# Kernel optimization log

Hardware: AMD Instinct MI355X
Metric: run time of the kernel (lower is better)

## Reference

```python
import jax, jax.numpy as jnp
import numpy as np

C = 1.0
TOP_K = 5
TAU = 0.1
NEG_SAMPLES = 20
EPS = 1e-9

B, D = 8192, 64


def setup_inputs() -> dict:
    key = jax.random.key(0)
    x = jax.random.normal(key, (B, D), dtype=jnp.float32)
    # scale into the Poincare ball (||x|| < 1)
    x = 0.9 * x / (1.0 + jnp.linalg.norm(x, axis=-1, keepdims=True))
    return {"embeds": x}


def _pairwise_poincare_distance(x):
    # ||xi - xj||^2 = ||xi||^2 + ||xj||^2 - 2 xi.xj  (same math as explicit diff,
    # avoids the [B,B,D] intermediate)
    norm_sq = jnp.sum(x * x, axis=-1)                      # [B]
    gram = x @ x.T                                          # [B,B]
    diff_norm_sq = jnp.maximum(norm_sq[:, None] + norm_sq[None, :] - 2.0 * gram, 0.0)
    ns_cl = jnp.minimum(norm_sq, 1.0 - EPS)
    denom = jnp.maximum((1.0 - ns_cl)[:, None] * (1.0 - ns_cl)[None, :], EPS)
    z = jnp.maximum(1.0 + 2.0 * diff_norm_sq / denom, 1.0 + EPS)
    return jnp.arccosh(z) / jnp.sqrt(jnp.float32(C))


def reference(embeds):
    n = embeds.shape[0]
    dist = _pairwise_poincare_distance(embeds)
    dist = jnp.where(jnp.eye(n, dtype=bool), jnp.inf, dist)

    k = min(TOP_K, n - 1)
    neg_vals, pos_idx = jax.lax.top_k(-dist, k)            # smallest k distances
    pos_dist = -neg_vals                                    # [B,k]
    pos_term = jax.nn.logsumexp(-pos_dist / TAU, axis=1)    # [B]

    rows = jnp.arange(n)[:, None]
    mask = jnp.ones((n, n), dtype=bool).at[rows, pos_idx].set(False)
    # indices of True (allowed) entries, per row; each row has exactly n-k True
    pool_idx = jnp.argsort(~mask, axis=1, stable=True)[:, : n - k]   # [B, n-k]

    skey = jax.random.key(42)
    samp = jax.random.randint(skey, (n, NEG_SAMPLES), 0, n - k)
    cols = jnp.take_along_axis(pool_idx, samp, axis=1)      # [B, neg_samples]
    neg_pool = jnp.take_along_axis(dist, cols, axis=1)      # [B, neg_samples]
    neg_term = jax.nn.logsumexp(-neg_pool / TAU, axis=1)    # [B]

    loss = -(pos_term - neg_term)
    return jnp.mean(loss)
```

## Files before the change

kernel.cpp:

```cpp
#include <hip/hip_runtime.h>
#include <cstdint>
#include <cstddef>

typedef _Float16 f16x8 __attribute__((ext_vector_type(8)));
typedef float f32x4 __attribute__((ext_vector_type(4)));

#define N_ROWS 8192
#define SPAN   8187u
#define MULT   1600u
#define TAU_INV 10.0f
#define TOTAL_SAMP 163840u
#define INIT32 0xFFFFFFFFu

__device__ __forceinline__ void tf_round(unsigned &x0, unsigned &x1, int r) {
    x0 += x1; x1 = (x1 << r) | (x1 >> (32 - r)); x1 ^= x0;
}
__device__ __forceinline__ void threefry2x32(unsigned k0, unsigned k1,
                                             unsigned c0, unsigned c1,
                                             unsigned &o0, unsigned &o1) {
    unsigned ks2 = k0 ^ k1 ^ 0x1BD11BDAu;
    unsigned x0 = c0 + k0, x1 = c1 + k1;
    tf_round(x0, x1, 13); tf_round(x0, x1, 15); tf_round(x0, x1, 26); tf_round(x0, x1, 6);
    x0 += k1;  x1 += ks2 + 1u;
    tf_round(x0, x1, 17); tf_round(x0, x1, 29); tf_round(x0, x1, 16); tf_round(x0, x1, 24);
    x0 += ks2; x1 += k0 + 2u;
    tf_round(x0, x1, 13); tf_round(x0, x1, 15); tf_round(x0, x1, 26); tf_round(x0, x1, 6);
    x0 += k0;  x1 += k1 + 3u;
    tf_round(x0, x1, 17); tf_round(x0, x1, 29); tf_round(x0, x1, 16); tf_round(x0, x1, 24);
    x0 += k1;  x1 += ks2 + 4u;
    tf_round(x0, x1, 13); tf_round(x0, x1, 15); tf_round(x0, x1, 26); tf_round(x0, x1, 6);
    x0 += ks2; x1 += k0 + 5u;
    o0 = x0; o1 = x1;
}

__device__ __forceinline__ void async16(void* lds, const void* g) {
    __builtin_amdgcn_global_load_lds((const __attribute__((address_space(1))) void*)g,
                                     (__attribute__((address_space(3))) void*)lds, 16, 0, 0);
}

__device__ __forceinline__ void stage_chunk(char* lds_tile, const char* gtile, int q, int lane) {
    int off16 = (q << 6) + lane;
    int r = off16 >> 3;
    int slot = off16 & 7;
    int csrc = slot ^ (r & 7);
    async16(lds_tile + (q << 10), gtile + r * 128 + (csrc << 4));
}

__device__ __forceinline__ f16x8 read_frag(const char* tile, int row, int c) {
    return *(const f16x8*)(tile + row * 128 + (((c ^ (row & 7)) << 4)));
}

__device__ __forceinline__ unsigned umed3(unsigned a, unsigned b, unsigned c) {
    unsigned d;
    asm("v_med3_u32 %0, %1, %2, %3" : "=v"(d) : "v"(a), "v"(b), "v"(c));
    return d;
}

__device__ __forceinline__ float wave_maxf(float v) {
#pragma unroll
    for (int o = 32; o; o >>= 1) v = fmaxf(v, __shfl_xor(v, o));
    return v;
}
__device__ __forceinline__ float wave_sumf(float v) {
#pragma unroll
    for (int o = 32; o; o >>= 1) v += __shfl_xor(v, o);
    return v;
}
__device__ __forceinline__ unsigned wave_minu32(unsigned v) {
#pragma unroll
    for (int o = 32; o; o >>= 1) {
        unsigned w = (unsigned)__shfl_xor((int)v, o);
        v = (w < v) ? w : v;
    }
    return v;
}
__device__ __forceinline__ unsigned group_minu32(unsigned v) {
#pragma unroll
    for (int o = 8; o; o >>= 1) {
        unsigned w = (unsigned)__shfl_xor((int)v, o);
        v = (w < v) ? w : v;
    }
    return v;
}

__global__ void prep_kernel(const float* __restrict__ X,
                            float2* __restrict__ nsiv,
                            char* __restrict__ Xf) {
    int t = blockIdx.x * 256 + threadIdx.x;
    int row = t >> 3, c = t & 7;
    const float4* src = (const float4*)(X + (size_t)row * 64 + c * 8);
    float4 a = src[0], b = src[1];
    float v[8] = {a.x, a.y, a.z, a.w, b.x, b.y, b.z, b.w};
    float ss = 0.f;
#pragma unroll
    for (int j = 0; j < 8; ++j) ss = fmaf(v[j], v[j], ss);
    ss += __shfl_xor(ss, 1);
    ss += __shfl_xor(ss, 2);
    ss += __shfl_xor(ss, 4);
    f16x8 h;
#pragma unroll
    for (int j = 0; j < 8; ++j) h[j] = (_Float16)v[j];
    *(f16x8*)(Xf + (size_t)row * 128 + c * 16) = h;
    if (c == 0) nsiv[row] = make_float2(ss, 1.0f / (1.0f - fminf(ss, 1.0f)));
}

__global__ __launch_bounds__(256, 3) void gram_topk(
        const char* __restrict__ Xf,
        const float2* __restrict__ nsiv, unsigned* __restrict__ part) {
    __shared__ __align__(16) char lds[16384];

    const int t = threadIdx.x, lane = t & 63, wv = t >> 6;
    const int lx = lane & 15, lq = lane >> 4;
    const int r0 = (blockIdx.x >> 5) * 128;
    const int ch = blockIdx.x & 31;
    const int j0base = ch * 256;

    const char* gA = Xf + (size_t)r0 * 128;
#pragma unroll
    for (int q = 0; q < 4; ++q) stage_chunk(lds, gA, 4 * wv + q, lane);
    __syncthreads();

    f16x8 a0f[2], a1f[2];
#pragma unroll
    for (int kc = 0; kc < 2; ++kc) {
        a0f[kc] = read_frag(lds, wv * 32 +      lx, kc * 4 + lq);
        a1f[kc] = read_frag(lds, wv * 32 + 16 + lx, kc * 4 + lq);
    }
    __syncthreads();

    stage_chunk(lds, Xf + (size_t)j0base * 128, 2 * wv, lane);
    stage_chunk(lds, Xf + (size_t)j0base * 128, 2 * wv + 1, lane);

    const char* pB0 = lds + lx * 128 + ((lq       ^ (lx & 7)) << 4);
    const char* pB1 = lds + lx * 128 + (((4 + lq) ^ (lx & 7)) << 4);
    const int rA  = 16 * wv + (lane >> 3);
    const int csA = (lane & 7) ^ ((lane >> 3) & 7);
    const char* gb = Xf + (size_t)(j0base + 64) * 128 + rA * 128 + (csA << 4);
    const float2* pn = nsiv + j0base + lx;
    const int jlx = j0base + lx;

    int gm0[4], gm1[4]; float rns0[4], rns1[4];
#pragma unroll
    for (int r = 0; r < 4; ++r) {
        int gr = r0 + wv * 32 + lq * 4 + r;
        gm0[r] = gr - jlx;
        gm1[r] = gr + 16 - jlx;
        rns0[r] = nsiv[gr].x;
        rns1[r] = nsiv[gr + 16].x;
    }

    unsigned tk0[4][5], tk1[4][5];
#pragma unroll
    for (int r = 0; r < 4; ++r)
#pragma unroll
        for (int s = 0; s < 5; ++s) { tk0[r][s] = INIT32; tk1[r][s] = INIT32; }

    int itofs = 0;
    __syncthreads();

#define INS5(TK, KK)                                                          \
    TK[4] = umed3(TK[3], TK[4], KK);                                          \
    TK[3] = umed3(TK[2], TK[3], KK);                                          \
    TK[2] = umed3(TK[1], TK[2], KK);                                          \
    TK[1] = umed3(TK[0], TK[1], KK);                                          \
    TK[0] = (KK < TK[0]) ? KK : TK[0];

#define ITER(SEL, NSEL, DO_STAGE) do {                                        \
    if (DO_STAGE) {                                                           \
        async16(lds + (NSEL) + wv * 2048,        gb);                         \
        async16(lds + (NSEL) + wv * 2048 + 1024, gb + 1024);                  \
        gb += 8192;                                                           \
    }                                                                         \
    float2 cnv[4] = {pn[0], pn[16], pn[32], pn[48]};                          \
    pn += 64;                                                                 \
    _Pragma("unroll")                                                         \
    for (int ct = 0; ct < 4; ++ct) {                                          \
        const f16x8 bh0 = *(const f16x8*)(pB0 + (SEL) + ct * 2048);           \
        const f16x8 bh1 = *(const f16x8*)(pB1 + (SEL) + ct * 2048);           \
        f32x4 a0 = {0.f, 0.f, 0.f, 0.f};                                      \
        f32x4 a1 = {0.f, 0.f, 0.f, 0.f};                                      \
        a0 = __builtin_amdgcn_mfma_f32_16x16x32_f16(a0f[0], bh0, a0, 0,0,0);  \
        a1 = __builtin_amdgcn_mfma_f32_16x16x32_f16(a1f[0], bh0, a1, 0,0,0);  \
        a0 = __builtin_amdgcn_mfma_f32_16x16x32_f16(a0f[1], bh1, a0, 0,0,0);  \
        a1 = __builtin_amdgcn_mfma_f32_16x16x32_f16(a1f[1], bh1, a1, 0,0,0);  \
        const float civ    = cnv[ct].y;                                       \
        const float cnsciv = cnv[ct].x * civ;                                 \
        const float m2civ  = -2.0f * civ;                                     \
        const unsigned gcol = (unsigned)(jlx + itofs + ct * 16);              \
        const int dofs = itofs + ct * 16;                                     \
        _Pragma("unroll")                                                     \
        for (int r = 0; r < 4; ++r) {                                         \
            float q0 = fmaf(a0[r], m2civ, fmaf(rns0[r], civ, cnsciv));        \
            q0 = fmaxf(q0, 0.0f);                                             \
            unsigned k0 = (__float_as_uint(q0) & 0xFFFFE000u) | gcol;         \
            k0 = (gm0[r] == dofs) ? INIT32 : k0;                              \
            INS5(tk0[r], k0)                                                  \
            float q1 = fmaf(a1[r], m2civ, fmaf(rns1[r], civ, cnsciv));        \
            q1 = fmaxf(q1, 0.0f);                                             \
            unsigned k1 = (__float_as_uint(q1) & 0xFFFFE000u) | gcol;         \
            k1 = (gm1[r] == dofs) ? INIT32 : k1;                              \
            INS5(tk1[r], k1)                                                  \
        }                                                                     \
    }                                                                         \
    itofs += 64;                                                              \
    __syncthreads();                                                          \
} while (0)

#pragma unroll 1
    for (int ip = 0; ip < 2; ++ip) {
        ITER(0, 8192, true);
        ITER(8192, 0, ip < 1);
    }
#undef ITER
#undef INS5

#define MERGE(TK, GM) do {                                                    \
    _Pragma("unroll")                                                         \
    for (int r = 0; r < 4; ++r) {                                             \
        unsigned t5r[5];                                                      \
        _Pragma("unroll")                                                     \
        for (int s = 0; s < 5; ++s) t5r[s] = TK[r][s];                        \
        unsigned out = INIT32;                                                \
        unsigned h = t5r[0];                                                  \
        _Pragma("unroll")                                                     \
        for (int s = 0; s < 5; ++s) {                                         \
            unsigned m = group_minu32(h);                                     \
            if (lx == s) out = m;                                             \
            if (h == m) {                                                     \
                t5r[0] = t5r[1]; t5r[1] = t5r[2]; t5r[2] = t5r[3];            \
                t5r[3] = t5r[4]; t5r[4] = INIT32;                             \
                h = t5r[0];                                                   \
            }                                                                 \
        }                                                                     \
        if (lx < 5) part[(size_t)(GM[r] + jlx) * 160 + (size_t)ch * 5 + lx] = out; \
    }                                                                         \
} while (0)

    MERGE(tk0, gm0);
    MERGE(tk1, gm1);
#undef MERGE
}

__global__ __launch_bounds__(256) void finalize_kernel(
        const float* __restrict__ X, const float2* __restrict__ nsiv,
        const unsigned* __restrict__ part, float* __restrict__ out) {
    const int t = threadIdx.x, lane = t & 63, wv = t >> 6;

    float wsum = 0.f;
#pragma unroll 1
    for (int rr = 0; rr < 4; ++rr) {
        const int row = blockIdx.x * 16 + wv * 4 + rr;

        const unsigned* prow = part + (size_t)row * 160;
        unsigned ka = prow[lane];
        unsigned kb = prow[64 + lane];
        unsigned kc = (lane < 32) ? prow[128 + lane] : INIT32;
        unsigned s0 = (ka < kb) ? ka : kb;
        unsigned s1 = (ka < kb) ? kb : ka;
        unsigned r0 = (s0 < kc) ? s0 : kc;
        unsigned tm = (s0 < kc) ? kc : s0;
        unsigned r1 = (s1 < tm) ? s1 : tm;
        unsigned r2 = (s1 < tm) ? tm : s1;
        unsigned b[5];
#pragma unroll
        for (int s = 0; s < 5; ++s) {
            unsigned m = wave_minu32(r0);
            b[s] = m;
            if (r0 == m) { r0 = r1; r1 = r2; r2 = INIT32; }
        }

        int pcol[5], ids[5];
#pragma unroll
        for (int s = 0; s < 5; ++s) { pcol[s] = (int)(b[s] & 8191u); ids[s] = pcol[s]; }
        for (int i = 0; i < 4; ++i)
            for (int j = 0; j < 4 - i; ++j)
                if (ids[j] > ids[j + 1]) { int tmp = ids[j]; ids[j] = ids[j + 1]; ids[j + 1] = tmp; }

        int col = row;
        if (lane < 20) {
            unsigned m0 = (unsigned)(row * 20 + lane);
            unsigned hi, lo;
            threefry2x32(0u, 42u, m0, m0 + TOTAL_SAMP, hi, lo);
            unsigned samp = ((hi % SPAN) * MULT + (lo % SPAN)) % SPAN;
            int c = (int)samp;
#pragma unroll
            for (int s = 0; s < 5; ++s) c += (ids[s] <= c) ? 1 : 0;
            col = c;
        } else if (lane < 25) {
            col = pcol[lane - 20];
        }

        float term = -INFINITY;
        if (lane < 25 && col != row) {
            const float4* xr = (const float4*)(X + (size_t)row * 64);
            const float4* xc = (const float4*)(X + (size_t)col * 64);
            float dot = 0.f;
#pragma unroll
            for (int k = 0; k < 16; ++k) {
                float4 a = xr[k];
                float4 c = xc[k];
                dot = fmaf(a.x, c.x, dot);
                dot = fmaf(a.y, c.y, dot);
                dot = fmaf(a.z, c.z, dot);
                dot = fmaf(a.w, c.w, dot);
            }
            float nsi = nsiv[row].x, nsj = nsiv[col].x;
            float d2  = fmaxf(nsi + nsj - 2.f * dot, 0.f);
            float ci  = 1.f - fminf(nsi, 1.f);
            float cj  = 1.f - fminf(nsj, 1.f);
            float den = fmaxf(ci * cj, 1e-9f);
            float z   = fmaxf(1.f + 2.f * d2 / den, 1.f);
            term = -acoshf(z) * TAU_INV;
        }

        float negt = (lane < 20) ? term : -INFINITY;
        float post = (lane >= 20 && lane < 25) ? term : -INFINITY;

        float nm = wave_maxf(negt);
        float ne = (lane < 20 && negt != -INFINITY) ? expf(negt - nm) : 0.f;
        float neg = nm + logf(wave_sumf(ne));

        float pm = wave_maxf(post);
        float pe = (lane >= 20 && lane < 25) ? expf(post - pm) : 0.f;
        float pos = pm + logf(wave_sumf(pe));

        if (lane == 0) wsum += neg - pos;
    }

    __shared__ float ws4[4];
    if (lane == 0) ws4[wv] = wsum;
    __syncthreads();
    if (t == 0)
        atomicAdd(out, (ws4[0] + ws4[1] + ws4[2] + ws4[3]) * (1.0f / 8192.0f));
}

extern "C" void kernel_launch(void* const* d_in, const int* in_sizes, int n_in,
                              void* d_out, int out_size, void* d_ws, size_t ws_size,
                              hipStream_t stream) {
    (void)in_sizes; (void)n_in; (void)out_size; (void)ws_size;
    const float* X = (const float*)d_in[0];
    float* out = (float*)d_out;

    float2*   nsiv = (float2*)d_ws;
    char*     Xf   = (char*)d_ws + 65536;
    unsigned* part = (unsigned*)((char*)d_ws + 65536 + 1048576);

    prep_kernel<<<256, 256, 0, stream>>>(X, nsiv, Xf);
    gram_topk<<<2048, 256, 0, stream>>>(Xf, nsiv, part);
    finalize_kernel<<<512, 256, 0, stream>>>(X, nsiv, part, out);
}
```

Baseline: 120.1 us.

## Specialize diagonal-free tiles and restructure finalize reduction with counter-based last-block write

The gram/top-k loop is split into two instantiations so that tiles not touching the diagonal skip the per-element self-distance masking compare. The finalize kernel now gives each wave one row in 1024-thread blocks instead of looping over four rows per wave in 256-thread blocks. It also replaces a direct atomicAdd into the output with partial sums spread over eight slots plus a completion counter, and the last block writes the mean. This removes the need for a pre-zeroed output and reduces atomic contention on one address, at the cost of zeroing workspace in the prep kernel and a threadfence handshake.

```diff
diff --git a/kernel.cpp b/kernel.cpp
--- a/kernel.cpp
+++ b/kernel.cpp
@@ -85,7 +85,13 @@
 
 __global__ void prep_kernel(const float* __restrict__ X,
                             float2* __restrict__ nsiv,
-                            char* __restrict__ Xf) {
+                            char* __restrict__ Xf,
+                            float* __restrict__ ws8,
+                            unsigned* __restrict__ cnt) {
+    if (blockIdx.x == 0 && threadIdx.x < 9) {
+        if (threadIdx.x < 8) ws8[threadIdx.x] = 0.f;
+        else *cnt = 0u;
+    }
     int t = blockIdx.x * 256 + threadIdx.x;
     int row = t >> 3, c = t & 7;
     const float4* src = (const float4*)(X + (size_t)row * 64 + c * 8);
@@ -165,7 +171,7 @@
     TK[1] = umed3(TK[0], TK[1], KK);                                          \
     TK[0] = (KK < TK[0]) ? KK : TK[0];
 
-#define ITER(SEL, NSEL, DO_STAGE) do {                                        \
+#define ITER(SEL, NSEL, DO_STAGE, DIAG) do {                                  \
     if (DO_STAGE) {                                                           \
         async16(lds + (NSEL) + wv * 2048,        gb);                         \
         async16(lds + (NSEL) + wv * 2048 + 1024, gb + 1024);                  \
@@ -188,17 +194,18 @@
         const float m2civ  = -2.0f * civ;                                     \
         const unsigned gcol = (unsigned)(jlx + itofs + ct * 16);              \
         const int dofs = itofs + ct * 16;                                     \
+        (void)dofs;                                                           \
         _Pragma("unroll")                                                     \
         for (int r = 0; r < 4; ++r) {                                         \
             float q0 = fmaf(a0[r], m2civ, fmaf(rns0[r], civ, cnsciv));        \
             q0 = fmaxf(q0, 0.0f);                                             \
             unsigned k0 = (__float_as_uint(q0) & 0xFFFFE000u) | gcol;         \
-            k0 = (gm0[r] == dofs) ? INIT32 : k0;                              \
+            if (DIAG) k0 = (gm0[r] == dofs) ? INIT32 : k0;                    \
             INS5(tk0[r], k0)                                                  \
             float q1 = fmaf(a1[r], m2civ, fmaf(rns1[r], civ, cnsciv));        \
             q1 = fmaxf(q1, 0.0f);                                             \
             unsigned k1 = (__float_as_uint(q1) & 0xFFFFE000u) | gcol;         \
-            k1 = (gm1[r] == dofs) ? INIT32 : k1;                              \
+            if (DIAG) k1 = (gm1[r] == dofs) ? INIT32 : k1;                    \
             INS5(tk1[r], k1)                                                  \
         }                                                                     \
     }                                                                         \
@@ -206,10 +213,19 @@
     __syncthreads();                                                          \
 } while (0)
 
+    const bool hasdiag = (r0 < j0base + 256) && (j0base < r0 + 128);
+    if (hasdiag) {
 #pragma unroll 1
-    for (int ip = 0; ip < 2; ++ip) {
-        ITER(0, 8192, true);
-        ITER(8192, 0, ip < 1);
+        for (int ip = 0; ip < 2; ++ip) {
+            ITER(0, 8192, true, 1);
+            ITER(8192, 0, ip < 1, 1);
+        }
+    } else {
+#pragma unroll 1
+        for (int ip = 0; ip < 2; ++ip) {
+            ITER(0, 8192, true, 0);
+            ITER(8192, 0, ip < 1, 0);
+        }
     }
 #undef ITER
 #undef INS5
@@ -241,97 +257,103 @@
 #undef MERGE
 }
 
-__global__ __launch_bounds__(256) void finalize_kernel(
+__global__ __launch_bounds__(1024) void finalize_kernel(
         const float* __restrict__ X, const float2* __restrict__ nsiv,
-        const unsigned* __restrict__ part, float* __restrict__ out) {
+        const unsigned* __restrict__ part, float* __restrict__ ws8,
+        unsigned* __restrict__ cnt, float* __restrict__ out) {
     const int t = threadIdx.x, lane = t & 63, wv = t >> 6;
-
-    float wsum = 0.f;
-#pragma unroll 1
-    for (int rr = 0; rr < 4; ++rr) {
-        const int row = blockIdx.x * 16 + wv * 4 + rr;
-
-        const unsigned* prow = part + (size_t)row * 160;
-        unsigned ka = prow[lane];
-        unsigned kb = prow[64 + lane];
-        unsigned kc = (lane < 32) ? prow[128 + lane] : INIT32;
-        unsigned s0 = (ka < kb) ? ka : kb;
-        unsigned s1 = (ka < kb) ? kb : ka;
-        unsigned r0 = (s0 < kc) ? s0 : kc;
-        unsigned tm = (s0 < kc) ? kc : s0;
-        unsigned r1 = (s1 < tm) ? s1 : tm;
-        unsigned r2 = (s1 < tm) ? tm : s1;
-        unsigned b[5];
-#pragma unroll
-        for (int s = 0; s < 5; ++s) {
-            unsigned m = wave_minu32(r0);
-            b[s] = m;
-            if (r0 == m) { r0 = r1; r1 = r2; r2 = INIT32; }
+    const int row = blockIdx.x * 16 + wv;
+
+    const unsigned* prow = part + (size_t)row * 160;
+    unsigned ka = prow[lane];
+    unsigned kb = prow[64 + lane];
+    unsigned kc = (lane < 32) ? prow[128 + lane] : INIT32;
+    unsigned s0 = (ka < kb) ? ka : kb;
+    unsigned s1 = (ka < kb) ? kb : ka;
+    unsigned r0 = (s0 < kc) ? s0 : kc;
+    unsigned tm = (s0 < kc) ? kc : s0;
+    unsigned r1 = (s1 < tm) ? s1 : tm;
+    unsigned r2 = (s1 < tm) ? tm : s1;
+    unsigned b[5];
+#pragma unroll
+    for (int s = 0; s < 5; ++s) {
+        unsigned m = wave_minu32(r0);
+        b[s] = m;
+        if (r0 == m) { r0 = r1; r1 = r2; r2 = INIT32; }
+    }
+
+    int pcol[5], ids[5];
+#pragma unroll
+    for (int s = 0; s < 5; ++s) { pcol[s] = (int)(b[s] & 8191u); ids[s] = pcol[s]; }
+    for (int i = 0; i < 4; ++i)
+        for (int j = 0; j < 4 - i; ++j)
+            if (ids[j] > ids[j + 1]) { int tmp = ids[j]; ids[j] = ids[j + 1]; ids[j + 1] = tmp; }
+
+    int col = row;
+    if (lane < 20) {
+        unsigned m0 = (unsigned)(row * 20 + lane);
+        unsigned hi, lo;
+        threefry2x32(0u, 42u, m0, m0 + TOTAL_SAMP, hi, lo);
+        unsigned samp = ((hi % SPAN) * MULT + (lo % SPAN)) % SPAN;
+        int c = (int)samp;
+#pragma unroll
+        for (int s = 0; s < 5; ++s) c += (ids[s] <= c) ? 1 : 0;
+        col = c;
+    } else if (lane < 25) {
+        col = pcol[lane - 20];
+    }
+
+    float term = -INFINITY;
+    if (lane < 25 && col != row) {
+        const float4* xr = (const float4*)(X + (size_t)row * 64);
+        const float4* xc = (const float4*)(X + (size_t)col * 64);
+        float dot = 0.f;
+#pragma unroll
+        for (int k = 0; k < 16; ++k) {
+            float4 a = xr[k];
+            float4 c = xc[k];
+            dot = fmaf(a.x, c.x, dot);
+            dot = fmaf(a.y, c.y, dot);
+            dot = fmaf(a.z, c.z, dot);
+            dot = fmaf(a.w, c.w, dot);
         }
-
-        int pcol[5], ids[5];
-#pragma unroll
-        for (int s = 0; s < 5; ++s) { pcol[s] = (int)(b[s] & 8191u); ids[s] = pcol[s]; }
-        for (int i = 0; i < 4; ++i)
-            for (int j = 0; j < 4 - i; ++j)
-                if (ids[j] > ids[j + 1]) { int tmp = ids[j]; ids[j] = ids[j + 1]; ids[j + 1] = tmp; }
-
-        int col = row;
-        if (lane < 20) {
-            unsigned m0 = (unsigned)(row * 20 + lane);
-            unsigned hi, lo;
-            threefry2x32(0u, 42u, m0, m0 + TOTAL_SAMP, hi, lo);
-            unsigned samp = ((hi % SPAN) * MULT + (lo % SPAN)) % SPAN;
-            int c = (int)samp;
-#pragma unroll
-            for (int s = 0; s < 5; ++s) c += (ids[s] <= c) ? 1 : 0;
-            col = c;
-        } else if (lane < 25) {
-            col = pcol[lane - 20];
+        float nsi = nsiv[row].x, nsj = nsiv[col].x;
+        float d2  = fmaxf(nsi + nsj - 2.f * dot, 0.f);
+        float ci  = 1.f - fminf(nsi, 1.f);
+        float cj  = 1.f - fminf(nsj, 1.f);
+        float den = fmaxf(ci * cj, 1e-9f);
+        float z   = fmaxf(1.f + 2.f * d2 / den, 1.f);
+        term = -acoshf(z) * TAU_INV;
+    }
+
+    float negt = (lane < 20) ? term : -INFINITY;
+    float post = (lane >= 20 && lane < 25) ? term : -INFINITY;
+
+    float nm = wave_maxf(negt);
+    float ne = (lane < 20 && negt != -INFINITY) ? expf(negt - nm) : 0.f;
+    float neg = nm + logf(wave_sumf(ne));
+
+    float pm = wave_maxf(post);
+    float pe = (lane >= 20 && lane < 25) ? expf(post - pm) : 0.f;
+    float pos = pm + logf(wave_sumf(pe));
+
+    __shared__ float ws16[16];
+    if (lane == 0) ws16[wv] = neg - pos;
+    __syncthreads();
+    if (t == 0) {
+        float s = 0.f;
+#pragma unroll
+        for (int i = 0; i < 16; ++i) s += ws16[i];
+        atomicAdd(&ws8[blockIdx.x & 7], s);
+        __threadfence();
+        unsigned old = atomicAdd(cnt, 1u);
+        if (old == 511u) {
+            float tot = 0.f;
+#pragma unroll
+            for (int i = 0; i < 8; ++i) tot += atomicAdd(&ws8[i], 0.0f);
+            out[0] = tot * (1.0f / 8192.0f);
         }
-
-        float term = -INFINITY;
-        if (lane < 25 && col != row) {
-            const float4* xr = (const float4*)(X + (size_t)row * 64);
-            const float4* xc = (const float4*)(X + (size_t)col * 64);
-            float dot = 0.f;
-#pragma unroll
-            for (int k = 0; k < 16; ++k) {
-                float4 a = xr[k];
-                float4 c = xc[k];
-                dot = fmaf(a.x, c.x, dot);
-                dot = fmaf(a.y, c.y, dot);
-                dot = fmaf(a.z, c.z, dot);
-                dot = fmaf(a.w, c.w, dot);
-            }
-            float nsi = nsiv[row].x, nsj = nsiv[col].x;
-            float d2  = fmaxf(nsi + nsj - 2.f * dot, 0.f);
-            float ci  = 1.f - fminf(nsi, 1.f);
-            float cj  = 1.f - fminf(nsj, 1.f);
-            float den = fmaxf(ci * cj, 1e-9f);
-            float z   = fmaxf(1.f + 2.f * d2 / den, 1.f);
-            term = -acoshf(z) * TAU_INV;
-        }
-
-        float negt = (lane < 20) ? term : -INFINITY;
-        float post = (lane >= 20 && lane < 25) ? term : -INFINITY;
-
-        float nm = wave_maxf(negt);
-        float ne = (lane < 20 && negt != -INFINITY) ? expf(negt - nm) : 0.f;
-        float neg = nm + logf(wave_sumf(ne));
-
-        float pm = wave_maxf(post);
-        float pe = (lane >= 20 && lane < 25) ? expf(post - pm) : 0.f;
-        float pos = pm + logf(wave_sumf(pe));
-
-        if (lane == 0) wsum += neg - pos;
-    }
-
-    __shared__ float ws4[4];
-    if (lane == 0) ws4[wv] = wsum;
-    __syncthreads();
-    if (t == 0)
-        atomicAdd(out, (ws4[0] + ws4[1] + ws4[2] + ws4[3]) * (1.0f / 8192.0f));
+    }
 }
 
 extern "C" void kernel_launch(void* const* d_in, const int* in_sizes, int n_in,
@@ -344,8 +366,10 @@
     float2*   nsiv = (float2*)d_ws;
     char*     Xf   = (char*)d_ws + 65536;
     unsigned* part = (unsigned*)((char*)d_ws + 65536 + 1048576);
-
-    prep_kernel<<<256, 256, 0, stream>>>(X, nsiv, Xf);
+    float*    ws8  = (float*)((char*)d_ws + 65536 + 1048576 + 5242880);
+    unsigned* cnt  = (unsigned*)((char*)d_ws + 65536 + 1048576 + 5242880 + 32);
+
+    prep_kernel<<<256, 256, 0, stream>>>(X, nsiv, Xf, ws8, cnt);
     gram_topk<<<2048, 256, 0, stream>>>(Xf, nsiv, part);
-    finalize_kernel<<<512, 256, 0, stream>>>(X, nsiv, part, out);
-}
+    finalize_kernel<<<512, 1024, 0, stream>>>(X, nsiv, part, ws8, cnt, out);
+}
```

Measured after the change: 126.8 us. +5.6%, slower.

## Triple-buffer column tiles, widen column chunks, and split final reduction into separate kernel

Applied to the files above, without the earlier changes.

The gram_topk kernel now gives each block 512 columns instead of 256, halving the grid and the partial top-k candidates per row (80 instead of 160). B tiles are staged through a three-buffer LDS ring with explicit vmcnt waits and raw barriers in place of the two-buffer __syncthreads scheme. Column norms are staged into LDS asynchronously. The finalize kernel uses one wave per row and writes per-row losses, and a new single-block reduce kernel replaces the atomicAdd. The goal is to hide global load latency and cut merge and finalize work, at the cost of more LDS per block, which may lower occupancy, and an extra kernel launch.

```diff
diff --git a/kernel.cpp b/kernel.cpp
--- a/kernel.cpp
+++ b/kernel.cpp
@@ -107,17 +107,19 @@
 __global__ __launch_bounds__(256, 3) void gram_topk(
         const char* __restrict__ Xf,
         const float2* __restrict__ nsiv, unsigned* __restrict__ part) {
-    __shared__ __align__(16) char lds[16384];
+    __shared__ __align__(16) char lds[29696];
 
     const int t = threadIdx.x, lane = t & 63, wv = t >> 6;
     const int lx = lane & 15, lq = lane >> 4;
-    const int r0 = (blockIdx.x >> 5) * 128;
-    const int ch = blockIdx.x & 31;
-    const int j0base = ch * 256;
+    const int r0 = (blockIdx.x >> 4) * 128;
+    const int ch = blockIdx.x & 15;
+    const int j0base = ch * 512;
 
     const char* gA = Xf + (size_t)r0 * 128;
 #pragma unroll
     for (int q = 0; q < 4; ++q) stage_chunk(lds, gA, 4 * wv + q, lane);
+    async16(lds + 24576 + wv * 1024, (const char*)(nsiv + j0base) + wv * 1024 + lane * 16);
+    if (wv == 0) async16(lds + 28672, (const char*)(nsiv + r0) + lane * 16);
     __syncthreads();
 
     f16x8 a0f[2], a1f[2];
@@ -126,28 +128,30 @@
         a0f[kc] = read_frag(lds, wv * 32 +      lx, kc * 4 + lq);
         a1f[kc] = read_frag(lds, wv * 32 + 16 + lx, kc * 4 + lq);
     }
+    const float2* rowns = (const float2*)(lds + 28672);
+    float rns0[4], rns1[4];
+#pragma unroll
+    for (int r = 0; r < 4; ++r) {
+        rns0[r] = rowns[wv * 32 + lq * 4 + r].x;
+        rns1[r] = rowns[wv * 32 + lq * 4 + r + 16].x;
+    }
+    const int jlx = j0base + lx;
+    const int dg  = (r0 + wv * 32 + lq * 4) - jlx;
     __syncthreads();
 
-    stage_chunk(lds, Xf + (size_t)j0base * 128, 2 * wv, lane);
-    stage_chunk(lds, Xf + (size_t)j0base * 128, 2 * wv + 1, lane);
-
-    const char* pB0 = lds + lx * 128 + ((lq       ^ (lx & 7)) << 4);
-    const char* pB1 = lds + lx * 128 + (((4 + lq) ^ (lx & 7)) << 4);
     const int rA  = 16 * wv + (lane >> 3);
     const int csA = (lane & 7) ^ ((lane >> 3) & 7);
-    const char* gb = Xf + (size_t)(j0base + 64) * 128 + rA * 128 + (csA << 4);
-    const float2* pn = nsiv + j0base + lx;
-    const int jlx = j0base + lx;
-
-    int gm0[4], gm1[4]; float rns0[4], rns1[4];
-#pragma unroll
-    for (int r = 0; r < 4; ++r) {
-        int gr = r0 + wv * 32 + lq * 4 + r;
-        gm0[r] = gr - jlx;
-        gm1[r] = gr + 16 - jlx;
-        rns0[r] = nsiv[gr].x;
-        rns1[r] = nsiv[gr + 16].x;
-    }
+    const char* gb = Xf + (size_t)j0base * 128 + rA * 128 + (csA << 4);
+    async16(lds +        wv * 2048,        gb);
+    async16(lds +        wv * 2048 + 1024, gb + 1024);
+    gb += 8192;
+    async16(lds + 8192 + wv * 2048,        gb);
+    async16(lds + 8192 + wv * 2048 + 1024, gb + 1024);
+    gb += 8192;
+
+    const char* pB0  = lds + lx * 128 + ((lq       ^ (lx & 7)) << 4);
+    const char* pB1  = lds + lx * 128 + (((4 + lq) ^ (lx & 7)) << 4);
+    const char* pnlp = lds + 24576 + lx * 8;
 
     unsigned tk0[4][5], tk1[4][5];
 #pragma unroll
@@ -156,7 +160,6 @@
         for (int s = 0; s < 5; ++s) { tk0[r][s] = INIT32; tk1[r][s] = INIT32; }
 
     int itofs = 0;
-    __syncthreads();
 
 #define INS5(TK, KK)                                                          \
     TK[4] = umed3(TK[3], TK[4], KK);                                          \
@@ -165,26 +168,31 @@
     TK[1] = umed3(TK[0], TK[1], KK);                                          \
     TK[0] = (KK < TK[0]) ? KK : TK[0];
 
-#define ITER(SEL, NSEL, DO_STAGE) do {                                        \
+#define ITER(RSEL, SSEL, DO_STAGE, VMSTR) do {                                \
+    asm volatile("" ::: "memory");                                            \
+    __builtin_amdgcn_s_barrier();      \
+    asm volatile("" ::: "memory");                                            \
     if (DO_STAGE) {                                                           \
-        async16(lds + (NSEL) + wv * 2048,        gb);                         \
-        async16(lds + (NSEL) + wv * 2048 + 1024, gb + 1024);                  \
+        async16(lds + (SSEL) + wv * 2048,        gb);                         \
+        async16(lds + (SSEL) + wv * 2048 + 1024, gb + 1024);                  \
         gb += 8192;                                                           \
     }                                                                         \
-    float2 cnv[4] = {pn[0], pn[16], pn[32], pn[48]};                          \
-    pn += 64;                                                                 \
+    asm volatile("s_waitcnt vmcnt(" VMSTR ")" ::: "memory");                  \
+    __builtin_amdgcn_s_barrier();      \
+    asm volatile("" ::: "memory");                                            \
     _Pragma("unroll")                                                         \
     for (int ct = 0; ct < 4; ++ct) {                                          \
-        const f16x8 bh0 = *(const f16x8*)(pB0 + (SEL) + ct * 2048);           \
-        const f16x8 bh1 = *(const f16x8*)(pB1 + (SEL) + ct * 2048);           \
+        const f16x8 bh0 = *(const f16x8*)(pB0 + (RSEL) + ct * 2048);          \
+        const f16x8 bh1 = *(const f16x8*)(pB1 + (RSEL) + ct * 2048);          \
         f32x4 a0 = {0.f, 0.f, 0.f, 0.f};                                      \
         f32x4 a1 = {0.f, 0.f, 0.f, 0.f};                                      \
         a0 = __builtin_amdgcn_mfma_f32_16x16x32_f16(a0f[0], bh0, a0, 0,0,0);  \
         a1 = __builtin_amdgcn_mfma_f32_16x16x32_f16(a1f[0], bh0, a1, 0,0,0);  \
         a0 = __builtin_amdgcn_mfma_f32_16x16x32_f16(a0f[1], bh1, a0, 0,0,0);  \
         a1 = __builtin_amdgcn_mfma_f32_16x16x32_f16(a1f[1], bh1, a1, 0,0,0);  \
-        const float civ    = cnv[ct].y;                                       \
-        const float cnsciv = cnv[ct].x * civ;                                 \
+        const float2 cn = *(const float2*)(pnlp + ct * 128);                  \
+        const float civ    = cn.y;                                            \
+        const float cnsciv = cn.x * civ;                                      \
         const float m2civ  = -2.0f * civ;                                     \
         const unsigned gcol = (unsigned)(jlx + itofs + ct * 16);              \
         const int dofs = itofs + ct * 16;                                     \
@@ -193,28 +201,32 @@
             float q0 = fmaf(a0[r], m2civ, fmaf(rns0[r], civ, cnsciv));        \
             q0 = fmaxf(q0, 0.0f);                                             \
             unsigned k0 = (__float_as_uint(q0) & 0xFFFFE000u) | gcol;         \
-            k0 = (gm0[r] == dofs) ? INIT32 : k0;                              \
+            k0 = (dofs - r == dg) ? INIT32 : k0;                              \
             INS5(tk0[r], k0)                                                  \
             float q1 = fmaf(a1[r], m2civ, fmaf(rns1[r], civ, cnsciv));        \
             q1 = fmaxf(q1, 0.0f);                                             \
             unsigned k1 = (__float_as_uint(q1) & 0xFFFFE000u) | gcol;         \
-            k1 = (gm1[r] == dofs) ? INIT32 : k1;                              \
+            k1 = (dofs - r - 16 == dg) ? INIT32 : k1;                         \
             INS5(tk1[r], k1)                                                  \
         }                                                                     \
     }                                                                         \
     itofs += 64;                                                              \
-    __syncthreads();                                                          \
+    pnlp  += 512;                                                             \
+    asm volatile("" ::: "memory");                                            \
 } while (0)
 
 #pragma unroll 1
     for (int ip = 0; ip < 2; ++ip) {
-        ITER(0, 8192, true);
-        ITER(8192, 0, ip < 1);
-    }
+        ITER(0,     16384, true, "4");
+        ITER(8192,  0,     true, "4");
+        ITER(16384, 8192,  true, "4");
+    }
+    ITER(0,    0, false, "2");
+    ITER(8192, 0, false, "0");
 #undef ITER
 #undef INS5
 
-#define MERGE(TK, GM) do {                                                    \
+#define MERGE(TK, ROWOFS) do {                                                \
     _Pragma("unroll")                                                         \
     for (int r = 0; r < 4; ++r) {                                             \
         unsigned t5r[5];                                                      \
@@ -232,106 +244,105 @@
                 h = t5r[0];                                                   \
             }                                                                 \
         }                                                                     \
-        if (lx < 5) part[(size_t)(GM[r] + jlx) * 160 + (size_t)ch * 5 + lx] = out; \
+        if (lx < 5)                                                           \
+            part[(size_t)(r0 + wv * 32 + lq * 4 + r + (ROWOFS)) * 80          \
+                 + (size_t)ch * 5 + lx] = out;                                \
     }                                                                         \
 } while (0)
 
-    MERGE(tk0, gm0);
-    MERGE(tk1, gm1);
+    MERGE(tk0, 0);
+    MERGE(tk1, 16);
 #undef MERGE
 }
 
 __global__ __launch_bounds__(256) void finalize_kernel(
         const float* __restrict__ X, const float2* __restrict__ nsiv,
-        const unsigned* __restrict__ part, float* __restrict__ out) {
+        const unsigned* __restrict__ part, float* __restrict__ rowloss) {
     const int t = threadIdx.x, lane = t & 63, wv = t >> 6;
-
-    float wsum = 0.f;
-#pragma unroll 1
-    for (int rr = 0; rr < 4; ++rr) {
-        const int row = blockIdx.x * 16 + wv * 4 + rr;
-
-        const unsigned* prow = part + (size_t)row * 160;
-        unsigned ka = prow[lane];
-        unsigned kb = prow[64 + lane];
-        unsigned kc = (lane < 32) ? prow[128 + lane] : INIT32;
-        unsigned s0 = (ka < kb) ? ka : kb;
-        unsigned s1 = (ka < kb) ? kb : ka;
-        unsigned r0 = (s0 < kc) ? s0 : kc;
-        unsigned tm = (s0 < kc) ? kc : s0;
-        unsigned r1 = (s1 < tm) ? s1 : tm;
-        unsigned r2 = (s1 < tm) ? tm : s1;
-        unsigned b[5];
-#pragma unroll
-        for (int s = 0; s < 5; ++s) {
-            unsigned m = wave_minu32(r0);
-            b[s] = m;
-            if (r0 == m) { r0 = r1; r1 = r2; r2 = INIT32; }
+    const int row = blockIdx.x * 4 + wv;
+
+    const unsigned* prow = part + (size_t)row * 80;
+    unsigned a0 = prow[lane];
+    unsigned a1 = (lane < 16) ? prow[64 + lane] : INIT32;
+    unsigned klo = (a0 < a1) ? a0 : a1;
+    unsigned khi = (a0 < a1) ? a1 : a0;
+    unsigned b[5];
+#pragma unroll
+    for (int s = 0; s < 5; ++s) {
+        unsigned m = wave_minu32(klo);
+        b[s] = m;
+        if (klo == m) { klo = khi; khi = INIT32; }
+    }
+
+    int pcol[5], ids[5];
+#pragma unroll
+    for (int s = 0; s < 5; ++s) { pcol[s] = (int)(b[s] & 8191u); ids[s] = pcol[s]; }
+    for (int i = 0; i < 4; ++i)
+        for (int j = 0; j < 4 - i; ++j)
+            if (ids[j] > ids[j + 1]) { int tmp = ids[j]; ids[j] = ids[j + 1]; ids[j + 1] = tmp; }
+
+    int col = row;
+    if (lane < 20) {
+        unsigned m0 = (unsigned)(row * 20 + lane);
+        unsigned hi, lo;
+        threefry2x32(0u, 42u, m0, m0 + TOTAL_SAMP, hi, lo);
+        unsigned samp = ((hi % SPAN) * MULT + (lo % SPAN)) % SPAN;
+        int c = (int)samp;
+#pragma unroll
+        for (int s = 0; s < 5; ++s) c += (ids[s] <= c) ? 1 : 0;
+        col = c;
+    } else if (lane < 25) {
+        col = pcol[lane - 20];
+    }
+
+    float term = -INFINITY;
+    if (lane < 25 && col != row) {
+        const float4* xr = (const float4*)(X + (size_t)row * 64);
+        const float4* xc = (const float4*)(X + (size_t)col * 64);
+        float dot = 0.f;
+#pragma unroll
+        for (int k = 0; k < 16; ++k) {
+            float4 a = xr[k];
+            float4 c = xc[k];
+            dot = fmaf(a.x, c.x, dot);
+            dot = fmaf(a.y, c.y, dot);
+            dot = fmaf(a.z, c.z, dot);
+            dot = fmaf(a.w, c.w, dot);
         }
-
-        int pcol[5], ids[5];
-#pragma unroll
-        for (int s = 0; s < 5; ++s) { pcol[s] = (int)(b[s] & 8191u); ids[s] = pcol[s]; }
-        for (int i = 0; i < 4; ++i)
-            for (int j = 0; j < 4 - i; ++j)
-                if (ids[j] > ids[j + 1]) { int tmp = ids[j]; ids[j] = ids[j + 1]; ids[j + 1] = tmp; }
-
-        int col = row;
-        if (lane < 20) {
-            unsigned m0 = (unsigned)(row * 20 + lane);
-            unsigned hi, lo;
-            threefry2x32(0u, 42u, m0, m0 + TOTAL_SAMP, hi, lo);
-            unsigned samp = ((hi % SPAN) * MULT + (lo % SPAN)) % SPAN;
-            int c = (int)samp;
-#pragma unroll
-            for (int s = 0; s < 5; ++s) c += (ids[s] <= c) ? 1 : 0;
-            col = c;
-        } else if (lane < 25) {
-            col = pcol[lane - 20];
-        }
-
-        float term = -INFINITY;
-        if (lane < 25 && col != row) {
-            const float4* xr = (const float4*)(X + (size_t)row * 64);
-            const float4* xc = (const float4*)(X + (size_t)col * 64);
-            float dot = 0.f;
-#pragma unroll
-            for (int k = 0; k < 16; ++k) {
-                float4 a = xr[k];
-                float4 c = xc[k];
-                dot = fmaf(a.x, c.x, dot);
-                dot = fmaf(a.y, c.y, dot);
-                dot = fmaf(a.z, c.z, dot);
-                dot = fmaf(a.w, c.w, dot);
-            }
-            float nsi = nsiv[row].x, nsj = nsiv[col].x;
-            float d2  = fmaxf(nsi + nsj - 2.f * dot, 0.f);
-            float ci  = 1.f - fminf(nsi, 1.f);
-            float cj  = 1.f - fminf(nsj, 1.f);
-            float den = fmaxf(ci * cj, 1e-9f);
-            float z   = fmaxf(1.f + 2.f * d2 / den, 1.f);
-            term = -acoshf(z) * TAU_INV;
-        }
-
-        float negt = (lane < 20) ? term : -INFINITY;
-        float post = (lane >= 20 && lane < 25) ? term : -INFINITY;
-
-        float nm = wave_maxf(negt);
-        float ne = (lane < 20 && negt != -INFINITY) ? expf(negt - nm) : 0.f;
-        float neg = nm + logf(wave_sumf(ne));
-
-        float pm = wave_maxf(post);
-        float pe = (lane >= 20 && lane < 25) ? expf(post - pm) : 0.f;
-        float pos = pm + logf(wave_sumf(pe));
-
-        if (lane == 0) wsum += neg - pos;
-    }
-
+        float nsi = nsiv[row].x, nsj = nsiv[col].x;
+        float d2  = fmaxf(nsi + nsj - 2.f * dot, 0.f);
+        float ci  = 1.f - fminf(nsi, 1.f);
+        float cj  = 1.f - fminf(nsj, 1.f);
+        float den = fmaxf(ci * cj, 1e-9f);
+        float z   = fmaxf(1.f + 2.f * d2 / den, 1.f);
+        term = -acoshf(z) * TAU_INV;
+    }
+
+    float negt = (lane < 20) ? term : -INFINITY;
+    float post = (lane >= 20 && lane < 25) ? term : -INFINITY;
+
+    float nm = wave_maxf(negt);
+    float ne = (lane < 20 && negt != -INFINITY) ? expf(negt - nm) : 0.f;
+    float neg = nm + logf(wave_sumf(ne));
+
+    float pm = wave_maxf(post);
+    float pe = (lane >= 20 && lane < 25) ? expf(post - pm) : 0.f;
+    float pos = pm + logf(wave_sumf(pe));
+
+    if (lane == 0) rowloss[row] = neg - pos;
+}
+
+__global__ void reduce_kernel(const float* __restrict__ rl, float* __restrict__ out) {
+    const int t = threadIdx.x;
+    float s = 0.f;
+#pragma unroll
+    for (int i = 0; i < 32; ++i) s += rl[t + 256 * i];
+#pragma unroll
+    for (int o = 32; o; o >>= 1) s += __shfl_xor(s, o);
     __shared__ float ws4[4];
-    if (lane == 0) ws4[wv] = wsum;
+    if ((t & 63) == 0) ws4[t >> 6] = s;
     __syncthreads();
-    if (t == 0)
-        atomicAdd(out, (ws4[0] + ws4[1] + ws4[2] + ws4[3]) * (1.0f / 8192.0f));
+    if (t == 0) out[0] = (ws4[0] + ws4[1] + ws4[2] + ws4[3]) * (1.0f / 8192.0f);
 }
 
 extern "C" void kernel_launch(void* const* d_in, const int* in_sizes, int n_in,
@@ -341,11 +352,13 @@
     const float* X = (const float*)d_in[0];
     float* out = (float*)d_out;
 
-    float2*   nsiv = (float2*)d_ws;
-    char*     Xf   = (char*)d_ws + 65536;
-    unsigned* part = (unsigned*)((char*)d_ws + 65536 + 1048576);
+    float2*   nsiv    = (float2*)d_ws;
+    char*     Xf      = (char*)d_ws + 65536;
+    unsigned* part    = (unsigned*)((char*)d_ws + 65536 + 1048576);
+    float*    rowloss = (float*)((char*)d_ws + 65536 + 1048576 + 2621440);
 
     prep_kernel<<<256, 256, 0, stream>>>(X, nsiv, Xf);
-    gram_topk<<<2048, 256, 0, stream>>>(Xf, nsiv, part);
-    finalize_kernel<<<512, 256, 0, stream>>>(X, nsiv, part, out);
-}
+    gram_topk<<<1024, 256, 0, stream>>>(Xf, nsiv, part);
+    finalize_kernel<<<2048, 256, 0, stream>>>(X, nsiv, part, rowloss);
+    reduce_kernel<<<1, 256, 0, stream>>>(rowloss, out);
+}
```

After: 104.6 us. 12.9% less time.
